# Kernel tuning notes

Hardware: AMD Instinct MI355X
Metric: run time of the kernel (lower is better)

The kernel has to match this reference:

```python
import jax, jax.numpy as jnp
import numpy as np

B, S, H, DH, HQ, HKV = 2, 1024, 2048, 128, 16, 4
E, K, I, IS = 16, 4, 1024, 1024
EPS = 1e-5
ROPE_BASE = 10000.0
ROUTED_SCALE = 1.0


def rmsnorm(x, w):
    v = jnp.mean(x.astype(jnp.float32) ** 2, axis=-1, keepdims=True)
    return (x.astype(jnp.float32) * jax.lax.rsqrt(v + EPS)).astype(x.dtype) * w


def rope(x, cos, sin):
    x1, x2 = jnp.split(x, 2, axis=-1)
    return jnp.concatenate([x1 * cos - x2 * sin, x2 * cos + x1 * sin], axis=-1)


def setup_inputs() -> dict:
    key = jax.random.key(0)
    ks = jax.random.split(key, 24)
    s = 0.02
    inp = {}
    inp['x'] = jax.random.normal(ks[0], (B, S, H), dtype=jnp.float32)
    inp['in_ln_w'] = jnp.ones((H,), jnp.float32)
    inp['wq'] = jax.random.normal(ks[1], (H, HQ * DH), jnp.float32) * s
    inp['bq'] = jax.random.normal(ks[2], (HQ * DH,), jnp.float32) * s
    inp['wk'] = jax.random.normal(ks[3], (H, HKV * DH), jnp.float32) * s
    inp['bk'] = jax.random.normal(ks[4], (HKV * DH,), jnp.float32) * s
    inp['wv'] = jax.random.normal(ks[5], (H, HKV * DH), jnp.float32) * s
    inp['bv'] = jax.random.normal(ks[6], (HKV * DH,), jnp.float32) * s
    inp['qn_w'] = jnp.ones((DH,), jnp.float32)
    inp['kn_w'] = jnp.ones((DH,), jnp.float32)
    inp['wo'] = jax.random.normal(ks[7], (HQ * DH, H), jnp.float32) * s
    inp['post_ln_w'] = jnp.ones((H,), jnp.float32)
    inp['gate_w'] = jax.random.normal(ks[8], (E, H), jnp.float32) * s
    inp['gate_b'] = jax.random.normal(ks[9], (E,), jnp.float32) * s
    inp['wg'] = jax.random.normal(ks[10], (E, H, I), jnp.float32) * s
    inp['wu'] = jax.random.normal(ks[11], (E, H, I), jnp.float32) * s
    inp['wd'] = jax.random.normal(ks[12], (E, I, H), jnp.float32) * s
    inp['swg'] = jax.random.normal(ks[13], (H, IS), jnp.float32) * s
    inp['swu'] = jax.random.normal(ks[14], (H, IS), jnp.float32) * s
    inp['swd'] = jax.random.normal(ks[15], (IS, H), jnp.float32) * s
    return inp


def reference(x, in_ln_w, wq, bq, wk, bk, wv, bv, qn_w, kn_w, wo, post_ln_w,
              gate_w, gate_b, wg, wu, wd, swg, swu, swd):
    # ---- attention block ----
    res = x
    h = rmsnorm(x, in_ln_w)
    q = (h @ wq + bq).reshape(B, S, HQ, DH)
    k = (h @ wk + bk).reshape(B, S, HKV, DH)
    v = (h @ wv + bv).reshape(B, S, HKV, DH)
    q = rmsnorm(q, qn_w)  # per-head QK norm over head_dim
    k = rmsnorm(k, kn_w)
    inv_freq = 1.0 / (ROPE_BASE ** (jnp.arange(0, DH, 2, dtype=jnp.float32) / DH))  # [DH/2]
    fr = jnp.arange(S, dtype=jnp.float32)[:, None] * inv_freq[None, :]  # [S, DH/2]
    cos = jnp.cos(fr)[None, :, None, :]
    sin = jnp.sin(fr)[None, :, None, :]
    q = rope(q, cos, sin)
    k = rope(k, cos, sin)
    g = HQ // HKV
    k = jnp.repeat(k, g, axis=2)  # GQA expand to [B,S,HQ,DH]
    v = jnp.repeat(v, g, axis=2)
    scores = jnp.einsum('bqhd,bkhd->bhqk', q, k) * (DH ** -0.5)
    causal = jnp.tril(jnp.ones((S, S), dtype=bool))
    scores = jnp.where(causal[None, None], scores, jnp.float32(-1e30))
    attn = jax.nn.softmax(scores, axis=-1)
    o = jnp.einsum('bhqk,bkhd->bqhd', attn, v).reshape(B, S, HQ * DH) @ wo
    x = res + o
    # ---- MoE block ----
    res = x
    h = rmsnorm(x, post_ln_w)
    ht = h.reshape(B * S, H)  # [T, H]
    logits = ht.astype(jnp.float32) @ gate_w.T  # fp32 router
    scr = jax.nn.sigmoid(logits)  # [T, E]
    choice = scr + gate_b[None, :]  # noaux_tc: bias only for selection
    _, topi = jax.lax.top_k(choice, K)  # [T, K]
    tw = jnp.take_along_axis(scr, topi, axis=-1)  # unbiased combine weights
    tw = tw / (jnp.sum(tw, axis=-1, keepdims=True) + 1e-20)  # norm_topk_prob
    tw = tw * ROUTED_SCALE
    cw = jnp.sum(jax.nn.one_hot(topi, E, dtype=jnp.float32) * tw[..., None], axis=1)  # [T, E]
    a = jnp.einsum('th,ehi->eti', ht, wg)
    b = jnp.einsum('th,ehi->eti', ht, wu)
    inter = jax.nn.silu(a) * b * cw.T[:, :, None]  # scale before down-proj
    routed = jnp.einsum('eti,eih->th', inter, wd)
    shared = (jax.nn.silu(ht @ swg) * (ht @ swu)) @ swd
    out = res + (routed + shared).reshape(B, S, H)
    return out
```

## Files before the change

kernel.cpp:

```cpp
#include <hip/hip_runtime.h>
#include <math.h>

typedef unsigned short u16;
typedef __attribute__((ext_vector_type(8))) short short8;
typedef __attribute__((ext_vector_type(4))) float f32x4;

#define B_ 2
#define S_ 1024
#define H_ 2048
#define DH_ 128
#define HQ_ 16
#define HKV_ 4
#define E_ 16
#define TOPK_ 4
#define I_ 1024
#define T_ (B_*S_)
#define NQKV_ 3072
#define NSEG_ 17
#define NA_ (T_*TOPK_ + T_)
#define K3_ 6144
#define MAXTILE 97

#define QPLANE ((long)B_*HQ_*S_*DH_)
#define KPLANE ((long)B_*HKV_*S_*DH_)
#define VPLANE ((long)B_*HKV_*DH_*S_)

__device__ __forceinline__ float bf2f(u16 u){
  union { unsigned int i; float f; } x; x.i = ((unsigned int)u) << 16; return x.f;
}
__device__ __forceinline__ u16 f2bf(float f){
  union { float f; unsigned int i; } x; x.f = f;
  unsigned int r = x.i + 0x7fffu + ((x.i >> 16) & 1u);
  return (u16)(r >> 16);
}
__device__ __forceinline__ void split_bf(float v, u16& hi, u16& lo){
  hi = f2bf(v);
  lo = f2bf(v - bf2f(hi));
}

__device__ __forceinline__ void gld_lds16(const void* g, void* l){
  __builtin_amdgcn_global_load_lds(
      (const __attribute__((address_space(1))) unsigned int*)g,
      (__attribute__((address_space(3))) unsigned int*)l, 16, 0, 0);
}

__device__ __forceinline__ f32x4 mfma_bf16(short8 a, short8 b, f32x4 c){
  return __builtin_amdgcn_mfma_f32_16x16x32_bf16(a, b, c, 0, 0, 0);
}

__global__ void k_transpose(const float* __restrict__ in, u16* __restrict__ out,
                            int R, int C, int rowMul, int rowOff,
                            long inBatch, long outBatch, int split3)
{
  __shared__ float tile[32][33];
  const float* inp = in + (long)blockIdx.z * inBatch;
  u16* outp = out + (long)blockIdx.z * outBatch;
  int c0 = blockIdx.x * 32, r0 = blockIdx.y * 32;
  int tx = threadIdx.x, ty = threadIdx.y;
#pragma unroll
  for (int i = 0; i < 4; i++)
    tile[ty*4+i][tx] = inp[(long)(r0 + ty*4 + i) * C + c0 + tx];
  __syncthreads();
#pragma unroll
  for (int i = 0; i < 4; i++){
    int c = c0 + ty*4 + i;
    float v = tile[tx][ty*4+i];
    if (split3){
      u16 hi, lo; split_bf(v, hi, lo);
      long base = (long)(c*rowMul + rowOff) * (3*R);
      outp[base + r0 + tx]       = hi;
      outp[base + R + r0 + tx]   = lo;
      outp[base + 2*R + r0 + tx] = hi;
    } else {
      outp[(long)(c*rowMul + rowOff) * R + r0 + tx] = f2bf(v);
    }
  }
}

__global__ void k_rmsnorm(const float* __restrict__ x, const float* __restrict__ w,
                          u16* __restrict__ out3)
{
  int t = blockIdx.x;
  const float4* r4 = (const float4*)(x + (long)t * H_);
  const float4* w4 = (const float4*)w;
  float4 a = r4[threadIdx.x], b = r4[threadIdx.x + 256];
  float ss = a.x*a.x + a.y*a.y + a.z*a.z + a.w*a.w
           + b.x*b.x + b.y*b.y + b.z*b.z + b.w*b.w;
#pragma unroll
  for (int d = 1; d < 64; d <<= 1) ss += __shfl_xor(ss, d);
  __shared__ float red[4];
  int lane = threadIdx.x & 63, wv = threadIdx.x >> 6;
  if (lane == 0) red[wv] = ss;
  __syncthreads();
  ss = red[0] + red[1] + red[2] + red[3];
  float rs = rsqrtf(ss * (1.f / 2048.f) + 1e-5f);
  float4 wa = w4[threadIdx.x], wb = w4[threadIdx.x + 256];
  float va[8] = { a.x*rs*wa.x, a.y*rs*wa.y, a.z*rs*wa.z, a.w*rs*wa.w,
                  b.x*rs*wb.x, b.y*rs*wb.y, b.z*rs*wb.z, b.w*rs*wb.w };
  int pos0 = threadIdx.x*4, pos1 = 1024 + threadIdx.x*4;
  ushort4 hi0, lo0, hi1, lo1;
  split_bf(va[0], hi0.x, lo0.x); split_bf(va[1], hi0.y, lo0.y);
  split_bf(va[2], hi0.z, lo0.z); split_bf(va[3], hi0.w, lo0.w);
  split_bf(va[4], hi1.x, lo1.x); split_bf(va[5], hi1.y, lo1.y);
  split_bf(va[6], hi1.z, lo1.z); split_bf(va[7], hi1.w, lo1.w);
  u16* row = out3 + (long)t * K3_;
  *(ushort4*)(row + pos0) = hi0;        *(ushort4*)(row + pos1) = hi1;
  *(ushort4*)(row + 2048 + pos0) = hi0; *(ushort4*)(row + 2048 + pos1) = hi1;
  *(ushort4*)(row + 4096 + pos0) = lo0; *(ushort4*)(row + 4096 + pos1) = lo1;
}

__global__ void k_add_rmsnorm(const float* __restrict__ x, const float* __restrict__ p0,
                              const float* __restrict__ w, float* __restrict__ xa,
                              u16* __restrict__ out1, float* __restrict__ outf)
{
  int t = blockIdx.x;
  long base = (long)t * H_;
  const float4* x4 = (const float4*)(x + base);
  const float4* a4 = (const float4*)(p0 + base);
  const float4* w4 = (const float4*)w;
  int i0 = threadIdx.x, i1 = threadIdx.x + 256;
  float4 xv0 = x4[i0], xv1 = x4[i1];
  float4 av0 = a4[i0], av1 = a4[i1];
  float4 s0, s1;
  s0.x = xv0.x+av0.x; s0.y = xv0.y+av0.y; s0.z = xv0.z+av0.z; s0.w = xv0.w+av0.w;
  s1.x = xv1.x+av1.x; s1.y = xv1.y+av1.y; s1.z = xv1.z+av1.z; s1.w = xv1.w+av1.w;
  *(float4*)(xa + base + i0*4) = s0;
  *(float4*)(xa + base + i1*4) = s1;
  float ss = s0.x*s0.x + s0.y*s0.y + s0.z*s0.z + s0.w*s0.w
           + s1.x*s1.x + s1.y*s1.y + s1.z*s1.z + s1.w*s1.w;
#pragma unroll
  for (int d = 1; d < 64; d <<= 1) ss += __shfl_xor(ss, d);
  __shared__ float red[4];
  int lane = threadIdx.x & 63, wv = threadIdx.x >> 6;
  if (lane == 0) red[wv] = ss;
  __syncthreads();
  ss = red[0] + red[1] + red[2] + red[3];
  float rs = rsqrtf(ss * (1.f / 2048.f) + 1e-5f);
  float4 wa = w4[i0], wb = w4[i1];
  float va[8] = { s0.x*rs*wa.x, s0.y*rs*wa.y, s0.z*rs*wa.z, s0.w*rs*wa.w,
                  s1.x*rs*wb.x, s1.y*rs*wb.y, s1.z*rs*wb.z, s1.w*rs*wb.w };
  ushort4 q0 = { f2bf(va[0]), f2bf(va[1]), f2bf(va[2]), f2bf(va[3]) };
  ushort4 q1 = { f2bf(va[4]), f2bf(va[5]), f2bf(va[6]), f2bf(va[7]) };
  *(ushort4*)(out1 + base + i0*4) = q0;
  *(ushort4*)(out1 + base + i1*4) = q1;
  float4 oa = { va[0], va[1], va[2], va[3] };
  float4 ob = { va[4], va[5], va[6], va[7] };
  *(float4*)(outf + base + i0*4) = oa;
  *(float4*)(outf + base + i1*4) = ob;
}

__global__ void k_ropetab(float* __restrict__ tab){
  int s = blockIdx.x, i = threadIdx.x;
  double inv = pow(10000.0, -(double)i / 64.0);
  double fr = (double)s * inv;
  tab[s*128 + i]      = (float)cos(fr);
  tab[s*128 + 64 + i] = (float)sin(fr);
}

__global__ void k_ropenorm(const float* __restrict__ qkv, const float* __restrict__ biascat,
                           const float* __restrict__ qnw, const float* __restrict__ knw,
                           const float* __restrict__ tab,
                           u16* __restrict__ Q, u16* __restrict__ Kn, u16* __restrict__ Vt)
{
  long gw = (long)blockIdx.x * 4 + (threadIdx.x >> 6);
  int lane = threadIdx.x & 63;
  int hr = (int)(gw % 24);
  long bs = gw / 24;
  int s = (int)(bs % S_);
  int b = (int)(bs / S_);
  long ro = bs * NQKV_ + hr * DH_;
  float x1 = qkv[ro + lane] + biascat[hr*DH_ + lane];
  float x2 = qkv[ro + lane + 64] + biascat[hr*DH_ + lane + 64];
  if (hr < 20){
    float ss = x1*x1 + x2*x2;
#pragma unroll
    for (int d = 1; d < 64; d <<= 1) ss += __shfl_xor(ss, d);
    float rs = rsqrtf(ss * (1.f/128.f) + 1e-5f);
    const float* wn = (hr < 16) ? qnw : knw;
    float y1 = x1 * rs * wn[lane], y2 = x2 * rs * wn[lane + 64];
    float c = tab[s*128 + lane], sn = tab[s*128 + 64 + lane];
    float o1 = y1*c - y2*sn, o2 = y2*c + y1*sn;
    if (hr < 16){
      const float sc = 0.088388347648318447f;
      u16 h1,l1,h2,l2;
      split_bf(o1*sc, h1, l1); split_bf(o2*sc, h2, l2);
      u16* dst = Q + (((long)b*HQ_ + hr)*S_ + s) * DH_;
      dst[lane] = h1; dst[lane+64] = h2;
      dst[QPLANE + lane] = l1; dst[QPLANE + lane+64] = l2;
    } else {
      u16 h1,l1,h2,l2;
      split_bf(o1, h1, l1); split_bf(o2, h2, l2);
      u16* dst = Kn + (((long)b*HKV_ + (hr-16))*S_ + s) * DH_;
      dst[lane] = h1; dst[lane+64] = h2;
      dst[KPLANE + lane] = l1; dst[KPLANE + lane+64] = l2;
    }
  } else {
    u16 h1,l1,h2,l2;
    split_bf(x1, h1, l1); split_bf(x2, h2, l2);
    u16* dst = Vt + (((long)b*HKV_ + (hr-20))*DH_) * S_ + s;
    dst[(long)lane * S_]        = h1;
    dst[(long)(lane + 64) * S_] = h2;
    dst[VPLANE + (long)lane * S_]        = l1;
    dst[VPLANE + (long)(lane + 64) * S_] = l2;
  }
}

__launch_bounds__(256)
__global__ void k_attn(const u16* __restrict__ Q, const u16* __restrict__ Kn,
                       const u16* __restrict__ Vt, u16* __restrict__ O3)
{
  __shared__ u16 Ksh[32][128];
  __shared__ u16 Ksl[32][128];
  __shared__ u16 Vsh[128][32];
  __shared__ u16 Vsl[128][32];
  __shared__ u16 Psh[4][16][40];
  __shared__ u16 Psl[4][16][40];
  int qb = blockIdx.x, h = blockIdx.y, b = blockIdx.z;
  int kvh = h >> 2;
  int q0 = qb * 64;
  int tid = threadIdx.x, lane = tid & 63, w = tid >> 6;

  const u16* Qg = Q  + (((long)b*HQ_  + h  )*S_ + q0) * DH_;
  const u16* Kg = Kn + (((long)b*HKV_ + kvh)*S_) * DH_;
  const u16* Vg = Vt + (((long)b*HKV_ + kvh)*DH_) * S_;

  short8 qh[4], ql[4];
  {
    long qrow = w*16 + (lane & 15);
    int coff = (lane >> 4) << 3;
#pragma unroll
    for (int kst = 0; kst < 4; kst++){
      qh[kst] = *(const short8*)(Qg + qrow*DH_ + kst*32 + coff);
      ql[kst] = *(const short8*)(Qg + QPLANE + qrow*DH_ + kst*32 + coff);
    }
  }

  f32x4 o[8];
#pragma unroll
  for (int nt = 0; nt < 8; nt++) o[nt] = (f32x4){0.f,0.f,0.f,0.f};
  float mrow[4] = {-INFINITY,-INFINITY,-INFINITY,-INFINITY};
  float lrow[4] = {0.f,0.f,0.f,0.f};

  for (int j = 0; j <= 2*qb + 1; ++j){
#pragma unroll
    for (int it = 0; it < 2; ++it){
      int flat = it*256 + tid;
      int r = flat >> 4, pc = flat & 15;
      int c = pc ^ (((r&7) << 1) | ((r >> 3) & 1));
      long gsrc = ((long)(j*32 + r))*DH_ + c*8;
      gld_lds16(Kg + gsrc,          &Ksh[0][0] + (it*256 + (w<<6))*8);
      gld_lds16(Kg + KPLANE + gsrc, &Ksl[0][0] + (it*256 + (w<<6))*8);
    }
#pragma unroll
    for (int it = 0; it < 2; ++it){
      int flat = it*256 + tid;
      int r = flat >> 2, pc = flat & 3;
      int c = pc ^ (r & 3);
      long gsrc = (long)r*S_ + j*32 + c*8;
      gld_lds16(Vg + gsrc,          &Vsh[0][0] + (it*256 + (w<<6))*8);
      gld_lds16(Vg + VPLANE + gsrc, &Vsl[0][0] + (it*256 + (w<<6))*8);
    }
    __syncthreads();

    f32x4 s[2];
#pragma unroll
    for (int nt = 0; nt < 2; nt++) s[nt] = (f32x4){0.f,0.f,0.f,0.f};
#pragma unroll
    for (int kst = 0; kst < 4; kst++){
#pragma unroll
      for (int nt = 0; nt < 2; nt++){
        int br = nt*16 + (lane & 15);
        int bc = (kst*4 + (lane >> 4)) ^ (((br&7)<<1) | ((br>>3)&1));
        short8 kh = *(const short8*)&Ksh[br][bc*8];
        short8 kl = *(const short8*)&Ksl[br][bc*8];
        s[nt] = mfma_bf16(qh[kst], kh, s[nt]);
        s[nt] = mfma_bf16(qh[kst], kl, s[nt]);
        s[nt] = mfma_bf16(ql[kst], kh, s[nt]);
      }
    }
    if (j >= 2*qb){
#pragma unroll
      for (int nt = 0; nt < 2; nt++){
        int key = j*32 + nt*16 + (lane & 15);
#pragma unroll
        for (int r = 0; r < 4; r++){
          int qrow = q0 + w*16 + ((lane >> 4) << 2) + r;
          if (key > qrow) s[nt][r] = -1e30f;
        }
      }
    }
    float pm[4];
#pragma unroll
    for (int r = 0; r < 4; r++) pm[r] = fmaxf(s[0][r], s[1][r]);
#pragma unroll
    for (int d = 1; d < 16; d <<= 1){
#pragma unroll
      for (int r = 0; r < 4; r++) pm[r] = fmaxf(pm[r], __shfl_xor(pm[r], d));
    }
    float alpha[4];
#pragma unroll
    for (int r = 0; r < 4; r++){
      float mn = fmaxf(mrow[r], pm[r]);
      alpha[r] = __expf(mrow[r] - mn);
      mrow[r] = mn;
    }
    float psum[4] = {0.f,0.f,0.f,0.f};
#pragma unroll
    for (int nt = 0; nt < 2; nt++){
#pragma unroll
      for (int r = 0; r < 4; r++){
        float p = __expf(s[nt][r] - mrow[r]);
        psum[r] += p;
        u16 ph, pl; split_bf(p, ph, pl);
        int qr = ((lane>>4)<<2) + r, kc = nt*16 + (lane & 15);
        Psh[w][qr][kc] = ph;
        Psl[w][qr][kc] = pl;
      }
    }
#pragma unroll
    for (int d = 1; d < 16; d <<= 1){
#pragma unroll
      for (int r = 0; r < 4; r++) psum[r] += __shfl_xor(psum[r], d);
    }
#pragma unroll
    for (int r = 0; r < 4; r++) lrow[r] = lrow[r]*alpha[r] + psum[r];
#pragma unroll
    for (int nt = 0; nt < 8; nt++)
#pragma unroll
      for (int r = 0; r < 4; r++) o[nt][r] *= alpha[r];

    {
      short8 pah = *(const short8*)&Psh[w][lane & 15][(lane >> 4) << 3];
      short8 pal = *(const short8*)&Psl[w][lane & 15][(lane >> 4) << 3];
#pragma unroll
      for (int nt = 0; nt < 8; nt++){
        int br = nt*16 + (lane & 15);
        int bc = (lane >> 4) ^ (br & 3);
        short8 vh = *(const short8*)&Vsh[br][bc*8];
        short8 vl = *(const short8*)&Vsl[br][bc*8];
        o[nt] = mfma_bf16(pah, vh, o[nt]);
        o[nt] = mfma_bf16(pah, vl, o[nt]);
        o[nt] = mfma_bf16(pal, vh, o[nt]);
      }
    }
    __syncthreads();
  }
  float inv_[4];
#pragma unroll
  for (int r = 0; r < 4; r++) inv_[r] = 1.f / lrow[r];
#pragma unroll
  for (int nt = 0; nt < 8; nt++){
#pragma unroll
    for (int r = 0; r < 4; r++){
      long row = (long)b*S_ + q0 + w*16 + ((lane >> 4) << 2) + r;
      float val = o[nt][r] * inv_[r];
      u16 hi, lo; split_bf(val, hi, lo);
      long base = row*K3_ + h*DH_ + nt*16 + (lane & 15);
      O3[base]        = hi;
      O3[base + 2048] = hi;
      O3[base + 4096] = lo;
    }
  }
}

template<int KITERS>
__launch_bounds__(256)
__global__ void k_gemm_d(const u16* __restrict__ A, const u16* __restrict__ Bm,
                         float* __restrict__ C, int N, int Kstride)
{
  __shared__ u16 LDS[4*8192];
  int tid = threadIdx.x;
  int lane = tid & 63, w = tid >> 6;
  int wr = w >> 1, wc = w & 1;
  int n0 = blockIdx.x * 128;
  int m0 = blockIdx.y * 128;

  const u16* aS[2]; const u16* bS[2];
#pragma unroll
  for (int it = 0; it < 2; ++it){
    int c = w + it*4;
    int row = c*16 + (lane >> 2);
    int ps = (lane & 3) ^ ((row >> 1) & 3);
    aS[it] = A + (long)(m0 + row) * Kstride + ps*8;
    bS[it] = Bm + (long)(n0 + row) * Kstride + ps*8;
  }

  int offA[4], offB[4];
#pragma unroll
  for (int m = 0; m < 4; m++){
    int r = wr*64 + m*16 + (lane & 15);
    int ps = (lane >> 4) ^ ((r >> 1) & 3);
    offA[m] = r*32 + ps*8;
  }
#pragma unroll
  for (int n = 0; n < 4; n++){
    int r = wc*64 + n*16 + (lane & 15);
    int ps = (lane >> 4) ^ ((r >> 1) & 3);
    offB[n] = 4096 + r*32 + ps*8;
  }

  f32x4 acc[4][4];
#pragma unroll
  for (int m = 0; m < 4; m++)
#pragma unroll
    for (int n = 0; n < 4; n++) acc[m][n] = (f32x4){0.f,0.f,0.f,0.f};

  auto STAGE = [&](int Tt){
    int kb = Tt * 32;
    int db = (Tt & 3) * 8192;
#pragma unroll
    for (int it = 0; it < 2; ++it){
      gld_lds16(aS[it] + kb, &LDS[db + (w + it*4)*512]);
      gld_lds16(bS[it] + kb, &LDS[db + 4096 + (w + it*4)*512]);
    }
  };

  STAGE(0); STAGE(1); STAGE(2);

  for (int T = 0; T < KITERS; ++T){
    if (T + 3 < KITERS) STAGE(T + 3);
    int rem = KITERS - 1 - T;
    if (rem >= 3)      asm volatile("s_waitcnt vmcnt(12)" ::: "memory");
    else if (rem == 2) asm volatile("s_waitcnt vmcnt(8)"  ::: "memory");
    else if (rem == 1) asm volatile("s_waitcnt vmcnt(4)"  ::: "memory");
    else               asm volatile("s_waitcnt vmcnt(0)"  ::: "memory");
    __builtin_amdgcn_s_barrier();
    __builtin_amdgcn_sched_barrier(0);
    const u16* L = &LDS[(T & 3) * 8192];
    short8 af[4], bfv[4];
#pragma unroll
    for (int m = 0; m < 4; m++) af[m]  = *(const short8*)(L + offA[m]);
#pragma unroll
    for (int n = 0; n < 4; n++) bfv[n] = *(const short8*)(L + offB[n]);
#pragma unroll
    for (int m = 0; m < 4; m++)
#pragma unroll
      for (int n = 0; n < 4; n++)
        acc[m][n] = mfma_bf16(af[m], bfv[n], acc[m][n]);
    asm volatile("s_waitcnt lgkmcnt(0)" ::: "memory");
    __builtin_amdgcn_sched_barrier(0);
    __builtin_amdgcn_s_barrier();
  }

#pragma unroll
  for (int m = 0; m < 4; m++){
    int row0 = m0 + wr*64 + m*16 + ((lane >> 4) << 2);
#pragma unroll
    for (int n = 0; n < 4; n++){
      int col = n0 + wc*64 + n*16 + (lane & 15);
#pragma unroll
      for (int r = 0; r < 4; r++)
        C[(long)(row0 + r)*N + col] = acc[m][n][r];
    }
  }
}

template<int MODE>
__launch_bounds__(256)
__global__ void k_gemm_g(const u16* __restrict__ A, const u16* __restrict__ Bm,
                         void* __restrict__ Cout,
                         int Kloop, long segStrideB,
                         const int* __restrict__ segStart, const int* __restrict__ segCount,
                         const int* __restrict__ tileSeg, const int* __restrict__ tileMb,
                         const int* __restrict__ meta,
                         const int* __restrict__ assignTS, const float* __restrict__ assignW,
                         u16* __restrict__ downb)
{
  __shared__ u16 As[128][64];
  __shared__ u16 Bs[128][64];
  int tid = threadIdx.x;
  int lane = tid & 63, w = tid >> 6;
  int wr = w >> 1, wc = w & 1;
  int n0 = blockIdx.x * 128;
  int ty = blockIdx.y;
  if (ty >= meta[0]) return;
  int seg = tileSeg[ty], m0 = tileMb[ty] * 128;
  int segBase = segStart[seg];
  int cnt = segCount[seg];
  const u16* Bp = Bm + (long)seg * segStrideB;

  const u16* aS[4]; const u16* bS[4];
#pragma unroll
  for (int it = 0; it < 4; ++it){
    int flat = it*256 + tid;
    int r = flat >> 3, pc = flat & 7;
    int c = pc ^ (r & 7);
    long arow;
    if constexpr (MODE == 2) arow = (long)(assignTS[segBase + m0 + r] >> 3);
    else arow = (long)(segBase + m0 + r);
    aS[it] = A + arow * Kloop + c*8;
    bS[it] = Bp + (long)(n0 + r) * Kloop + c*8;
  }

  f32x4 acc[4][4];
#pragma unroll
  for (int m = 0; m < 4; m++)
#pragma unroll
    for (int n = 0; n < 4; n++) acc[m][n] = (f32x4){0.f,0.f,0.f,0.f};

  u16* AsF = &As[0][0]; u16* BsF = &Bs[0][0];
  for (int k0 = 0; k0 < Kloop; k0 += 64){
#pragma unroll
    for (int it = 0; it < 4; ++it){
      gld_lds16(aS[it] + k0, AsF + (it*256 + (w<<6))*8);
      gld_lds16(bS[it] + k0, BsF + (it*256 + (w<<6))*8);
    }
    __syncthreads();
#pragma unroll
    for (int kh = 0; kh < 2; ++kh){
      short8 af[4], bfv[4];
#pragma unroll
      for (int m = 0; m < 4; m++){
        int r = wr*64 + m*16 + (lane & 15);
        int c = (kh*4 + (lane >> 4)) ^ (r & 7);
        af[m] = *(const short8*)&As[r][c*8];
      }
#pragma unroll
      for (int n = 0; n < 4; n++){
        int r = wc*64 + n*16 + (lane & 15);
        int c = (kh*4 + (lane >> 4)) ^ (r & 7);
        bfv[n] = *(const short8*)&Bs[r][c*8];
      }
#pragma unroll
      for (int m = 0; m < 4; m++)
#pragma unroll
        for (int n = 0; n < 4; n++)
          acc[m][n] = mfma_bf16(af[m], bfv[n], acc[m][n]);
    }
    __syncthreads();
  }

  if constexpr (MODE == 2){
    u16* inter = (u16*)Cout;
#pragma unroll
    for (int m = 0; m < 4; m++){
      int row0 = m0 + wr*64 + m*16 + ((lane >> 4) << 2);
#pragma unroll
      for (int n = 0; n < 4; n++){
        f32x4 a = acc[m][n];
        float ov[4];
#pragma unroll
        for (int r = 0; r < 4; r++) ov[r] = __shfl_xor(a[r], 1);
        if ((lane & 1) == 0){
          int colp = (n0 + wc*64 + n*16 + (lane & 15)) >> 1;
#pragma unroll
          for (int r = 0; r < 4; r++){
            int rl = row0 + r;
            if (rl < cnt){
              int pos = segBase + rl;
              float g = a[r], u = ov[r];
              float val = (g / (1.f + __expf(-g))) * u * assignW[pos];
              inter[(long)pos*I_ + colp] = f2bf(val);
            }
          }
        }
      }
    }
  } else {
#pragma unroll
    for (int m = 0; m < 4; m++){
      int row0 = m0 + wr*64 + m*16 + ((lane >> 4) << 2);
#pragma unroll
      for (int n = 0; n < 4; n++){
        int col = n0 + wc*64 + n*16 + (lane & 15);
#pragma unroll
        for (int r = 0; r < 4; r++){
          int rl = row0 + r;
          if (rl < cnt){
            int ts = assignTS[segBase + rl];
            downb[((long)(ts >> 3)*5 + (ts & 7))*H_ + col] = f2bf(acc[m][n][r]);
          }
        }
      }
    }
  }
}

__global__ void k_router(const float* __restrict__ ht, const float* __restrict__ gw,
                         const float* __restrict__ gb, int* __restrict__ tok_e,
                         float* __restrict__ tok_w, int* __restrict__ counts)
{
  int t = blockIdx.x * 4 + (threadIdx.x >> 6);
  int lane = threadIdx.x & 63;
  const float4* row4 = (const float4*)(ht + (long)t * H_);
  float acc[16];
#pragma unroll
  for (int e = 0; e < 16; e++) acc[e] = 0.f;
#pragma unroll
  for (int it = 0; it < 8; it++){
    float4 rv = row4[lane + 64*it];
#pragma unroll
    for (int e = 0; e < 16; e++){
      float4 gv = *(const float4*)(gw + (long)e*H_ + (lane + 64*it)*4);
      acc[e] += rv.x*gv.x + rv.y*gv.y + rv.z*gv.z + rv.w*gv.w;
    }
  }
#pragma unroll
  for (int d = 1; d < 64; d <<= 1){
#pragma unroll
    for (int e = 0; e < 16; e++) acc[e] += __shfl_xor(acc[e], d);
  }
  if (lane == 0){
    float scr[16], ch[16];
#pragma unroll
    for (int e = 0; e < 16; e++){
      float s = 1.f / (1.f + __expf(-acc[e]));
      scr[e] = s; ch[e] = s + gb[e];
    }
    int sel[4]; float tw[4]; float sum = 0.f;
#pragma unroll
    for (int k = 0; k < 4; k++){
      int best = -1; float bv = -1e30f;
      for (int e = 0; e < 16; e++){
        bool used = false;
        for (int j = 0; j < k; j++) if (sel[j] == e) used = true;
        if (!used && ch[e] > bv){ bv = ch[e]; best = e; }
      }
      sel[k] = best; tw[k] = scr[best]; sum += scr[best];
    }
    float inv = 1.f / (sum + 1e-20f);
#pragma unroll
    for (int k = 0; k < 4; k++){
      tok_e[t*4 + k] = sel[k];
      tok_w[t*4 + k] = tw[k] * inv;
      atomicAdd(&counts[sel[k]], 1);
    }
  }
}

__global__ void k_scan(const int* __restrict__ counts, int* __restrict__ segStart,
                       int* __restrict__ segCount, int* __restrict__ cursor,
                       int* __restrict__ tileSeg, int* __restrict__ tileMb,
                       int* __restrict__ meta)
{
  if (threadIdx.x == 0){
    int off = 0, nt = 0;
    for (int e = 0; e < 16; e++){
      segStart[e] = off; segCount[e] = counts[e]; cursor[e] = off;
      for (int mb = 0; mb*128 < counts[e]; ++mb){ tileSeg[nt] = e; tileMb[nt] = mb; nt++; }
      off += counts[e];
    }
    segStart[16] = T_*TOPK_; segCount[16] = T_;
    for (int mb = 0; mb < 16; ++mb){ tileSeg[nt] = 16; tileMb[nt] = mb; nt++; }
    meta[0] = nt;
  }
}

__global__ void k_scatter(const int* __restrict__ tok_e, const float* __restrict__ tok_w,
                          int* __restrict__ cursor, int* __restrict__ assignTS,
                          float* __restrict__ assignW)
{
  int t = blockIdx.x*256 + threadIdx.x;
  if (t < T_){
    for (int k = 0; k < 4; k++){
      int e = tok_e[t*4 + k];
      int pos = atomicAdd(&cursor[e], 1);
      assignTS[pos] = t*8 + k;
      assignW[pos] = tok_w[t*4 + k];
    }
    assignTS[T_*TOPK_ + t] = t*8 + 4;
    assignW[T_*TOPK_ + t] = 1.f;
  }
}

__global__ void k_final(const float* __restrict__ xa, const u16* __restrict__ downb,
                        float* __restrict__ out)
{
  long i = ((long)blockIdx.x*256 + threadIdx.x) * 4;
  int t = (int)(i >> 11);
  int h = (int)(i & 2047);
  float4 r = *(const float4*)(xa + i);
  float a0 = r.x, a1 = r.y, a2 = r.z, a3 = r.w;
#pragma unroll
  for (int k = 0; k < 5; k++){
    const u16* d = downb + ((long)t*5 + k)*H_ + h;
    ushort4 v = *(const ushort4*)d;
    a0 += bf2f(v.x); a1 += bf2f(v.y); a2 += bf2f(v.z); a3 += bf2f(v.w);
  }
  float4 o = { a0, a1, a2, a3 };
  *(float4*)(out + i) = o;
}

extern "C" void kernel_launch(void* const* d_in, const int* in_sizes, int n_in,
                              void* d_out, int out_size, void* d_ws, size_t ws_size,
                              hipStream_t stream)
{
  (void)in_sizes; (void)n_in; (void)out_size; (void)ws_size;
  const float* x      = (const float*)d_in[0];
  const float* inlnw  = (const float*)d_in[1];
  const float* wq     = (const float*)d_in[2];
  const float* bq     = (const float*)d_in[3];
  const float* wk     = (const float*)d_in[4];
  const float* bk     = (const float*)d_in[5];
  const float* wv     = (const float*)d_in[6];
  const float* bv     = (const float*)d_in[7];
  const float* qnw    = (const float*)d_in[8];
  const float* knw    = (const float*)d_in[9];
  const float* wo     = (const float*)d_in[10];
  const float* postln = (const float*)d_in[11];
  const float* gatew  = (const float*)d_in[12];
  const float* gateb  = (const float*)d_in[13];
  const float* wg     = (const float*)d_in[14];
  const float* wu     = (const float*)d_in[15];
  const float* wdp    = (const float*)d_in[16];
  const float* swg    = (const float*)d_in[17];
  const float* swu    = (const float*)d_in[18];
  const float* swd    = (const float*)d_in[19];
  float* out = (float*)d_out;

  char* ws = (char*)d_ws;
  size_t off = 0;
  auto alloc = [&](size_t bytes) -> char* {
    char* p = ws + off; off += (bytes + 255) & ~(size_t)255; return p;
  };
  u16*   wqkv2   = (u16*)  alloc((size_t)NQKV_*K3_*2);
  u16*   wo2     = (u16*)  alloc((size_t)H_*K3_*2);
  u16*   wgu_t   = (u16*)  alloc((size_t)NSEG_*2048*2048*2);
  u16*   wd_t    = (u16*)  alloc((size_t)NSEG_*2048*1024*2);
  float* tab     = (float*)alloc((size_t)S_*128*4);
  float* biascat = (float*)alloc((size_t)NQKV_*4);
  float* xa      = (float*)alloc((size_t)T_*H_*4);
  int*   tok_e   = (int*)  alloc((size_t)T_*4*4);
  float* tok_w   = (float*)alloc((size_t)T_*4*4);
  int*   counts  = (int*)  alloc(32*4);
  int*   segStart= (int*)  alloc(32*4);
  int*   segCount= (int*)  alloc(32*4);
  int*   cursor  = (int*)  alloc(32*4);
  int*   tileSeg = (int*)  alloc(128*4);
  int*   tileMb  = (int*)  alloc(128*4);
  int*   meta    = (int*)  alloc(32*4);
  int*   assignTS= (int*)  alloc((size_t)NA_*4);
  float* assignW = (float*)alloc((size_t)NA_*4);
  char*  scrA    = alloc((size_t)T_*K3_*2);
  char*  scrBC   = alloc((size_t)2*T_*NQKV_*4);
  char*  scrD    = alloc((size_t)(2*QPLANE + 2*KPLANE + 2*VPLANE)*2);

  u16*   h2      = (u16*)scrA;
  u16*   attno2  = (u16*)scrA;
  u16*   inter   = (u16*)scrA;
  float* qkvp0   = (float*)scrBC;
  float* wop     = (float*)scrBC;
  u16*   Qb2     = (u16*)scrD;
  u16*   Kn2     = (u16*)(scrD + (size_t)2*QPLANE*2);
  u16*   Vt2     = (u16*)(scrD + (size_t)2*QPLANE*2 + (size_t)2*KPLANE*2);
  float* ht_f    = (float*)scrD;
  u16*   ht_b    = (u16*)(scrD + (size_t)T_*H_*4);
  u16*   downb   = (u16*)scrD;

  dim3 tb(32, 8);
  k_transpose<<<dim3(64,64,1),  tb, 0, stream>>>(wq,  wqkv2, 2048, 2048, 1, 0,    0, 0, 1);
  k_transpose<<<dim3(16,64,1),  tb, 0, stream>>>(wk,  wqkv2, 2048, 512,  1, 2048, 0, 0, 1);
  k_transpose<<<dim3(16,64,1),  tb, 0, stream>>>(wv,  wqkv2, 2048, 512,  1, 2560, 0, 0, 1);
  k_transpose<<<dim3(64,64,1),  tb, 0, stream>>>(wo,  wo2,   2048, 2048, 1, 0,    0, 0, 1);
  k_transpose<<<dim3(32,64,16), tb, 0, stream>>>(wg,  wgu_t, 2048, 1024, 2, 0, (long)2048*1024, (long)2048*2048, 0);
  k_transpose<<<dim3(32,64,16), tb, 0, stream>>>(wu,  wgu_t, 2048, 1024, 2, 1, (long)2048*1024, (long)2048*2048, 0);
  k_transpose<<<dim3(32,64,1),  tb, 0, stream>>>(swg, wgu_t + (long)16*2048*2048, 2048, 1024, 2, 0, 0, 0, 0);
  k_transpose<<<dim3(32,64,1),  tb, 0, stream>>>(swu, wgu_t + (long)16*2048*2048, 2048, 1024, 2, 1, 0, 0, 0);
  k_transpose<<<dim3(64,32,16), tb, 0, stream>>>(wdp, wd_t,  1024, 2048, 1, 0, (long)1024*2048, (long)2048*1024, 0);
  k_transpose<<<dim3(64,32,1),  tb, 0, stream>>>(swd, wd_t + (long)16*2048*1024, 1024, 2048, 1, 0, 0, 0, 0);

  hipMemcpyAsync(biascat,        bq, 2048*4, hipMemcpyDeviceToDevice, stream);
  hipMemcpyAsync(biascat + 2048, bk, 512*4,  hipMemcpyDeviceToDevice, stream);
  hipMemcpyAsync(biascat + 2560, bv, 512*4,  hipMemcpyDeviceToDevice, stream);

  k_ropetab<<<S_, 64, 0, stream>>>(tab);
  k_rmsnorm<<<T_, 256, 0, stream>>>(x, inlnw, h2);

  k_gemm_d<192><<<dim3(24,16), 256, 0, stream>>>(h2, wqkv2, qkvp0, NQKV_, K3_);

  k_ropenorm<<<(T_*24)/4, 256, 0, stream>>>(qkvp0, biascat, qnw, knw, tab, Qb2, Kn2, Vt2);

  k_attn<<<dim3(S_/64, HQ_, B_), 256, 0, stream>>>(Qb2, Kn2, Vt2, attno2);

  k_gemm_d<192><<<dim3(16,16), 256, 0, stream>>>(attno2, wo2, wop, H_, K3_);

  k_add_rmsnorm<<<T_, 256, 0, stream>>>(x, wop, postln, xa, ht_b, ht_f);

  hipMemsetAsync(counts, 0, 32*4, stream);
  k_router<<<T_/4, 256, 0, stream>>>(ht_f, gatew, gateb, tok_e, tok_w, counts);
  k_scan<<<1, 64, 0, stream>>>(counts, segStart, segCount, cursor, tileSeg, tileMb, meta);
  k_scatter<<<(T_+255)/256, 256, 0, stream>>>(tok_e, tok_w, cursor, assignTS, assignW);

  k_gemm_g<2><<<dim3(16,MAXTILE), 256, 0, stream>>>(ht_b, wgu_t, inter,
      H_, (long)2048*2048, segStart, segCount, tileSeg, tileMb, meta, assignTS, assignW, nullptr);

  k_gemm_g<3><<<dim3(16,MAXTILE), 256, 0, stream>>>(inter, wd_t, nullptr,
      I_, (long)2048*1024, segStart, segCount, tileSeg, tileMb, meta, assignTS, assignW, downb);

  k_final<<<(T_*H_/4)/256, 256, 0, stream>>>(xa, downb, out);
}
```

Baseline: 858.1 us.

## Triple-buffer grouped MoE GEMM loads and swizzle dense GEMM block order

The grouped expert GEMM (gate/up and down projections) now uses a three-stage LDS ring with a K-step of 32 and asynchronous global-to-LDS loads issued two steps ahead. It uses vmcnt waits instead of a full __syncthreads around each 64-wide tile. This mirrors the pipeline already used in the dense GEMM and is meant to hide global memory latency behind MFMA work. Separately, the dense GEMM remaps block IDs in groups of 8 to improve L2 locality. The changes add more barriers per K and raise LDS use, and the swizzle assumes the workgroup count is divisible by 8.

```diff
diff --git a/kernel.cpp b/kernel.cpp
--- a/kernel.cpp
+++ b/kernel.cpp
@@ -372,8 +372,13 @@
   int tid = threadIdx.x;
   int lane = tid & 63, w = tid >> 6;
   int wr = w >> 1, wc = w & 1;
-  int n0 = blockIdx.x * 128;
-  int m0 = blockIdx.y * 128;
+  int nbx = gridDim.x;
+  int nwg = nbx * gridDim.y;
+  int id = blockIdx.y * nbx + blockIdx.x;
+  int cpx = nwg >> 3;
+  int swz = (id & 7) * cpx + (id >> 3);
+  int n0 = (swz % nbx) * 128;
+  int m0 = (swz / nbx) * 128;
 
   const u16* aS[2]; const u16* bS[2];
 #pragma unroll
@@ -455,19 +460,18 @@
   }
 }
 
-template<int MODE>
+template<int MODE, int KITERS>
 __launch_bounds__(256)
 __global__ void k_gemm_g(const u16* __restrict__ A, const u16* __restrict__ Bm,
                          void* __restrict__ Cout,
-                         int Kloop, long segStrideB,
+                         int Kstride, long segStrideB,
                          const int* __restrict__ segStart, const int* __restrict__ segCount,
                          const int* __restrict__ tileSeg, const int* __restrict__ tileMb,
                          const int* __restrict__ meta,
                          const int* __restrict__ assignTS, const float* __restrict__ assignW,
                          u16* __restrict__ downb)
 {
-  __shared__ u16 As[128][64];
-  __shared__ u16 Bs[128][64];
+  __shared__ u16 LDS[3*8192];
   int tid = threadIdx.x;
   int lane = tid & 63, w = tid >> 6;
   int wr = w >> 1, wc = w & 1;
@@ -479,17 +483,31 @@
   int cnt = segCount[seg];
   const u16* Bp = Bm + (long)seg * segStrideB;
 
-  const u16* aS[4]; const u16* bS[4];
-#pragma unroll
-  for (int it = 0; it < 4; ++it){
-    int flat = it*256 + tid;
-    int r = flat >> 3, pc = flat & 7;
-    int c = pc ^ (r & 7);
+  const u16* aS[2]; const u16* bS[2];
+#pragma unroll
+  for (int it = 0; it < 2; ++it){
+    int c = w + it*4;
+    int row = c*16 + (lane >> 2);
+    int ps = (lane & 3) ^ ((row >> 1) & 3);
     long arow;
-    if constexpr (MODE == 2) arow = (long)(assignTS[segBase + m0 + r] >> 3);
-    else arow = (long)(segBase + m0 + r);
-    aS[it] = A + arow * Kloop + c*8;
-    bS[it] = Bp + (long)(n0 + r) * Kloop + c*8;
+    if constexpr (MODE == 2) arow = (long)(assignTS[segBase + m0 + row] >> 3);
+    else arow = (long)(segBase + m0 + row);
+    aS[it] = A + arow * Kstride + ps*8;
+    bS[it] = Bp + (long)(n0 + row) * Kstride + ps*8;
+  }
+
+  int offA[4], offB[4];
+#pragma unroll
+  for (int m = 0; m < 4; m++){
+    int r = wr*64 + m*16 + (lane & 15);
+    int ps = (lane >> 4) ^ ((r >> 1) & 3);
+    offA[m] = r*32 + ps*8;
+  }
+#pragma unroll
+  for (int n = 0; n < 4; n++){
+    int r = wc*64 + n*16 + (lane & 15);
+    int ps = (lane >> 4) ^ ((r >> 1) & 3);
+    offB[n] = 4096 + r*32 + ps*8;
   }
 
   f32x4 acc[4][4];
@@ -498,36 +516,40 @@
 #pragma unroll
     for (int n = 0; n < 4; n++) acc[m][n] = (f32x4){0.f,0.f,0.f,0.f};
 
-  u16* AsF = &As[0][0]; u16* BsF = &Bs[0][0];
-  for (int k0 = 0; k0 < Kloop; k0 += 64){
-#pragma unroll
-    for (int it = 0; it < 4; ++it){
-      gld_lds16(aS[it] + k0, AsF + (it*256 + (w<<6))*8);
-      gld_lds16(bS[it] + k0, BsF + (it*256 + (w<<6))*8);
-    }
-    __syncthreads();
-#pragma unroll
-    for (int kh = 0; kh < 2; ++kh){
-      short8 af[4], bfv[4];
-#pragma unroll
-      for (int m = 0; m < 4; m++){
-        int r = wr*64 + m*16 + (lane & 15);
-        int c = (kh*4 + (lane >> 4)) ^ (r & 7);
-        af[m] = *(const short8*)&As[r][c*8];
-      }
-#pragma unroll
-      for (int n = 0; n < 4; n++){
-        int r = wc*64 + n*16 + (lane & 15);
-        int c = (kh*4 + (lane >> 4)) ^ (r & 7);
-        bfv[n] = *(const short8*)&Bs[r][c*8];
-      }
-#pragma unroll
-      for (int m = 0; m < 4; m++)
-#pragma unroll
-        for (int n = 0; n < 4; n++)
-          acc[m][n] = mfma_bf16(af[m], bfv[n], acc[m][n]);
-    }
-    __syncthreads();
+  auto STAGE = [&](int Tt){
+    int kb = Tt * 32;
+    int db = (Tt % 3) * 8192;
+#pragma unroll
+    for (int it = 0; it < 2; ++it){
+      gld_lds16(aS[it] + kb, &LDS[db + (w + it*4)*512]);
+      gld_lds16(bS[it] + kb, &LDS[db + 4096 + (w + it*4)*512]);
+    }
+  };
+
+  STAGE(0); STAGE(1);
+
+  for (int T = 0; T < KITERS; ++T){
+    if (T + 2 < KITERS) STAGE(T + 2);
+    int rem = KITERS - 1 - T;
+    if (rem >= 2)      asm volatile("s_waitcnt vmcnt(8)" ::: "memory");
+    else if (rem == 1) asm volatile("s_waitcnt vmcnt(4)" ::: "memory");
+    else               asm volatile("s_waitcnt vmcnt(0)" ::: "memory");
+    __builtin_amdgcn_s_barrier();
+    __builtin_amdgcn_sched_barrier(0);
+    const u16* L = &LDS[(T % 3) * 8192];
+    short8 af[4], bfv[4];
+#pragma unroll
+    for (int m = 0; m < 4; m++) af[m]  = *(const short8*)(L + offA[m]);
+#pragma unroll
+    for (int n = 0; n < 4; n++) bfv[n] = *(const short8*)(L + offB[n]);
+#pragma unroll
+    for (int m = 0; m < 4; m++)
+#pragma unroll
+      for (int n = 0; n < 4; n++)
+        acc[m][n] = mfma_bf16(af[m], bfv[n], acc[m][n]);
+    asm volatile("s_waitcnt lgkmcnt(0)" ::: "memory");
+    __builtin_amdgcn_sched_barrier(0);
+    __builtin_amdgcn_s_barrier();
   }
 
   if constexpr (MODE == 2){
@@ -781,10 +803,10 @@
   k_scan<<<1, 64, 0, stream>>>(counts, segStart, segCount, cursor, tileSeg, tileMb, meta);
   k_scatter<<<(T_+255)/256, 256, 0, stream>>>(tok_e, tok_w, cursor, assignTS, assignW);
 
-  k_gemm_g<2><<<dim3(16,MAXTILE), 256, 0, stream>>>(ht_b, wgu_t, inter,
+  k_gemm_g<2,64><<<dim3(16,MAXTILE), 256, 0, stream>>>(ht_b, wgu_t, inter,
       H_, (long)2048*2048, segStart, segCount, tileSeg, tileMb, meta, assignTS, assignW, nullptr);
 
-  k_gemm_g<3><<<dim3(16,MAXTILE), 256, 0, stream>>>(inter, wd_t, nullptr,
+  k_gemm_g<3,32><<<dim3(16,MAXTILE), 256, 0, stream>>>(inter, wd_t, nullptr,
       I_, (long)2048*1024, segStart, segCount, tileSeg, tileMb, meta, assignTS, assignW, downb);
 
   k_final<<<(T_*H_/4)/256, 256, 0, stream>>>(xa, downb, out);
```

Result: slower. 898.7 us (+4.7%).
